# Kernel tuning notes

Hardware: AMD Instinct MI355X
Metric: run time of the kernel (lower is better)

## Reference

```python
import jax, jax.numpy as jnp
import numpy as np

KSIZE = 3
STRIDE = 1
PADDING = 1
DILATION = 1
C_IN = 16
C_OUT = 16


def setup_inputs() -> dict:
    key = jax.random.key(0)
    k1, k2, k3 = jax.random.split(key, 3)
    inputs = jax.random.normal(k1, (2, C_IN, 24, 24, 24, 24), dtype=jnp.float32)
    weight = jax.random.normal(k2, (C_OUT, C_IN * KSIZE ** 4), dtype=jnp.float32)
    bias = jax.random.normal(k3, (1, C_OUT, 1, 1, 1, 1), dtype=jnp.float32)
    return {"inputs": inputs, "weight": weight, "bias": bias}


def reference(inputs, weight, bias):
    # weight stored flattened: [C_out, C_in * k^4] -> [C_out, C_in, k, k, k, k]
    w = weight.reshape(C_OUT, C_IN, KSIZE, KSIZE, KSIZE, KSIZE)
    # General 4-spatial-dim convolution via XLA's ND conv.
    dn = jax.lax.ConvDimensionNumbers(
        lhs_spec=(0, 1, 2, 3, 4, 5),   # N, C, U, V, H, W
        rhs_spec=(0, 1, 2, 3, 4, 5),   # O, I, kU, kV, kH, kW
        out_spec=(0, 1, 2, 3, 4, 5),
    )
    out = jax.lax.conv_general_dilated(
        inputs, w,
        window_strides=(STRIDE,) * 4,
        padding=((PADDING, PADDING),) * 4,
        rhs_dilation=(DILATION,) * 4,
        dimension_numbers=dn,
    )
    return out + bias
```

## Files before the change

### kernel.cpp

```cpp
#include <hip/hip_runtime.h>

#define S 24
#define PLANE 576
#define CISTRIDE 331776
#define SLAB_B 21632
#define QBUF_B 6144
#define QOFF 3328
#define A_BYTES 46080
#define WS_SLABS A_BYTES

typedef __attribute__((ext_vector_type(8))) short bf16x8;
typedef __attribute__((ext_vector_type(4))) float f32x4;

__device__ __forceinline__ ushort f2bf(float f) {
    unsigned int u = __builtin_bit_cast(unsigned int, f);
    unsigned int r = u + 0x7fffu + ((u >> 16) & 1u);
    return (ushort)(r >> 16);
}

__global__ void __launch_bounds__(256)
pack_in(const float* __restrict__ in, const float* __restrict__ wgt, char* __restrict__ ws) {
    __shared__ __align__(16) float lds_f[16 * 576];

    const int b = blockIdx.x;
    const int nb = b / PLANE, uv = b % PLANE;
    const float* src = in + (size_t)nb * 16 * CISTRIDE + (size_t)uv * PLANE;
    char* dst = ws + WS_SLABS + (size_t)b * SLAB_B;
    const int t = threadIdx.x;

    #pragma unroll
    for (int r = 0; r < 9; ++r) {
        int chunk = r * 256 + t;
        int ci = chunk / 144, q4 = chunk % 144;
        __builtin_amdgcn_global_load_lds(
            (const __attribute__((address_space(1))) unsigned int*)(src + (size_t)ci * CISTRIDE + 4 * q4),
            (__attribute__((address_space(3))) unsigned int*)(&lds_f[chunk * 4]),
            16, 0, 0);
    }
    __syncthreads();

    #pragma unroll
    for (int i = 0; i < 6; ++i) {
        int c = i * 256 + t;
        if (c < 1352) {
            int pos = c >> 1, h = c & 1;
            int row = pos / 26, col = pos % 26;
            uint4 o = make_uint4(0, 0, 0, 0);
            if (row >= 1 && row <= 24 && col >= 1 && col <= 24) {
                int q = (row - 1) * 24 + (col - 1);
                #pragma unroll
                for (int kk = 0; kk < 4; ++kk) {
                    float fa = lds_f[(8 * h + 2 * kk) * 576 + q];
                    float fb = lds_f[(8 * h + 2 * kk + 1) * 576 + q];
                    ((unsigned*)&o)[kk] = (unsigned)f2bf(fa) | ((unsigned)f2bf(fb) << 16);
                }
            }
            *(uint4*)(dst + (((size_t)c * 16) ^ (size_t)((row & 3) << 4))) = o;
        }
    }

    if (b == 0) {
        for (int i = t; i < 2880; i += 256) {
            int step = i >> 6;
            int tap = step / 5, s = step % 5;
            int lane = i & 63;
            int co = lane & 15, gA = lane >> 4;
            int o = 2 * s + (gA >> 1);
            int cib = (gA & 1) * 8;
            ushort vals[8];
            #pragma unroll
            for (int j = 0; j < 8; ++j)
                vals[j] = (o <= 8) ? f2bf(wgt[co * 1296 + (cib + j) * 81 + tap * 9 + o]) : (ushort)0;
            uint4 pk;
            pk.x = vals[0] | ((unsigned)vals[1] << 16);
            pk.y = vals[2] | ((unsigned)vals[3] << 16);
            pk.z = vals[4] | ((unsigned)vals[5] << 16);
            pk.w = vals[6] | ((unsigned)vals[7] << 16);
            *(uint4*)(ws + (size_t)i * 16) = pk;
        }
    }
}

__global__ void __launch_bounds__(192, 4)
conv4d_main(const char* __restrict__ ws, const float* __restrict__ bias,
            float* __restrict__ out) {
    __shared__ __align__(16) char lds[2 * QBUF_B];

    const int t = threadIdx.x, lane = t & 63, wvid = t >> 6;
    const int braw = blockIdx.x;
    const int b = (braw & 7) * 216 + (braw >> 3);
    const int nb = b / 864, rem = b % 864;
    const int u = rem / 36, rem2 = rem % 36;
    const int v0 = (rem2 / 6) * 4, qq = rem2 % 6;

    const int n16 = lane & 15, g = lane >> 4;
    const int dh = n16 >> 3, dw = n16 & 7;
    const int half = g & 1, osel = g >> 1;

    int loff[2][5];
    #pragma unroll
    for (int tr = 0; tr < 2; ++tr)
        #pragma unroll
        for (int s = 0; s < 5; ++s) {
            int o = 2 * s + osel; if (o > 8) o = 8;
            int kh = o / 3, kw = o % 3;
            int r_off = dh + kh, c_off = dw + kw;
            int lin = (r_off * 26 + c_off) * 32 + half * 16;
            loff[tr][s] = lin ^ (((tr * 2 + r_off) & 3) << 4);
        }

    f32x4 acc[4][2];
    #pragma unroll
    for (int a = 0; a < 4; ++a)
        #pragma unroll
        for (int tr = 0; tr < 2; ++tr) acc[a][tr] = (f32x4){0, 0, 0, 0};

    unsigned mask = 0;
    #pragma unroll
    for (int i = 0; i < 18; ++i) {
        int uu = u + i / 6 - 1, vv = v0 + i % 6 - 1;
        if (uu >= 0 && uu < S && vv >= 0 && vv < S) mask |= 1u << i;
    }

    const char* slabs = ws + WS_SLABS;
    const size_t qoff = (size_t)qq * QOFF;
    #define SPTR(w_) (slabs + ((size_t)nb * PLANE                                        \
        + (size_t)min(max(u + (w_) / 6 - 1, 0), 23) * S                                  \
        + (size_t)min(max(v0 + (w_) % 6 - 1, 0), 23)) * SLAB_B + qoff)

    #define STAGE(bufsel_, src_) do {                                                    \
        const char* _s = (src_);                                                         \
        _Pragma("unroll")                                                                \
        for (int r2 = 0; r2 < 2; ++r2) {                                                 \
            int chunk = r2 * 192 + t;                                                    \
            __builtin_amdgcn_global_load_lds(                                            \
                (const __attribute__((address_space(1))) unsigned int*)(_s + (size_t)chunk * 16), \
                (__attribute__((address_space(3))) unsigned int*)(lds + (bufsel_) * QBUF_B + chunk * 16), \
                16, 0, 0);                                                               \
        }                                                                                \
    } while (0)

    STAGE(0, SPTR(0));
    STAGE(1, SPTR(1));

    bf16x8 afr[3][5];

    #pragma unroll
    for (int w = 0; w < 18; ++w) {
        if (w <= 16) asm volatile("s_waitcnt vmcnt(2)" ::: "memory");
        else         asm volatile("s_waitcnt vmcnt(0)" ::: "memory");
        __builtin_amdgcn_s_barrier();

        if ((w % 6) == 0) {
            const int ku = w / 6;
            #pragma unroll
            for (int kv = 0; kv < 3; ++kv) {
                const char* ap = ws + (size_t)(ku * 3 + kv) * 5120 + (size_t)lane * 16;
                #pragma unroll
                for (int s = 0; s < 5; ++s) afr[kv][s] = *(const bf16x8*)(ap + s * 1024);
            }
        }

        if (mask & (1u << w)) {
            const int vj = w % 6;
            const char* bp = lds + (w & 1) * QBUF_B + wvid * 256;
            #pragma unroll
            for (int tr = 0; tr < 2; ++tr) {
                #pragma unroll
                for (int s = 0; s < 5; ++s) {
                    bf16x8 bfr = *(const bf16x8*)(bp + tr * 1664 + loff[tr][s]);
                    #pragma unroll
                    for (int kv = 0; kv < 3; ++kv) {
                        const int a = vj - kv;
                        if (a >= 0 && a <= 3)
                            acc[a][tr] = __builtin_amdgcn_mfma_f32_16x16x32_bf16(afr[kv][s], bfr, acc[a][tr], 0, 0, 0);
                    }
                }
            }
        }
        __builtin_amdgcn_s_barrier();
        if (w + 2 < 18) STAGE(w & 1, SPTR(w + 2));
    }

    float bv[4];
    #pragma unroll
    for (int r = 0; r < 4; ++r) bv[r] = bias[g * 4 + r];
    #pragma unroll
    for (int a = 0; a < 4; ++a) {
        float* outp = out + (size_t)nb * 16 * CISTRIDE + (size_t)(u * S + v0 + a) * PLANE;
        #pragma unroll
        for (int tr = 0; tr < 2; ++tr) {
            int row = qq * 4 + tr * 2 + dh;
            int col = wvid * 8 + dw;
            int pos = row * S + col;
            #pragma unroll
            for (int r = 0; r < 4; ++r)
                outp[(size_t)(g * 4 + r) * CISTRIDE + pos] = acc[a][tr][r] + bv[r];
        }
    }
}

extern "C" void kernel_launch(void* const* d_in, const int* in_sizes, int n_in,
                              void* d_out, int out_size, void* d_ws, size_t ws_size,
                              hipStream_t stream) {
    const float* in   = (const float*)d_in[0];
    const float* wgt  = (const float*)d_in[1];
    const float* bias = (const float*)d_in[2];
    float* out        = (float*)d_out;
    char* ws          = (char*)d_ws;

    pack_in<<<dim3(1152), dim3(256), 0, stream>>>(in, wgt, ws);
    conv4d_main<<<dim3(1728), dim3(192), 0, stream>>>(ws, bias, out);
}
```

Measured before the change: 68.83 us.

## Fuse input bf16 packing into conv kernel, loading fp32 directly via registers

Drops the separate input-packing pass that wrote padded, swizzled bf16 slabs to workspace. The conv kernel now loads fp32 input straight from global memory into registers one window ahead, converts to bf16, writes the swizzled LDS tile itself and zero-fills the halo border. Only a tiny single-block kernel still packs the weights. This removes a full read-and-write pass over the input and one launch. In exchange the main kernel reads twice the bytes per element, prefetches only one stage ahead, and carries more registers.

```diff
diff --git a/kernel.cpp b/kernel.cpp
--- a/kernel.cpp
+++ b/kernel.cpp
@@ -3,11 +3,8 @@
 #define S 24
 #define PLANE 576
 #define CISTRIDE 331776
-#define SLAB_B 21632
-#define QBUF_B 6144
-#define QOFF 3328
+#define BUF_B 4992
 #define A_BYTES 46080
-#define WS_SLABS A_BYTES
 
 typedef __attribute__((ext_vector_type(8))) short bf16x8;
 typedef __attribute__((ext_vector_type(4))) float f32x4;
@@ -19,72 +16,32 @@
 }
 
 __global__ void __launch_bounds__(256)
-pack_in(const float* __restrict__ in, const float* __restrict__ wgt, char* __restrict__ ws) {
-    __shared__ __align__(16) float lds_f[16 * 576];
-
-    const int b = blockIdx.x;
-    const int nb = b / PLANE, uv = b % PLANE;
-    const float* src = in + (size_t)nb * 16 * CISTRIDE + (size_t)uv * PLANE;
-    char* dst = ws + WS_SLABS + (size_t)b * SLAB_B;
+pack_w(const float* __restrict__ wgt, char* __restrict__ ws) {
     const int t = threadIdx.x;
-
-    #pragma unroll
-    for (int r = 0; r < 9; ++r) {
-        int chunk = r * 256 + t;
-        int ci = chunk / 144, q4 = chunk % 144;
-        __builtin_amdgcn_global_load_lds(
-            (const __attribute__((address_space(1))) unsigned int*)(src + (size_t)ci * CISTRIDE + 4 * q4),
-            (__attribute__((address_space(3))) unsigned int*)(&lds_f[chunk * 4]),
-            16, 0, 0);
-    }
-    __syncthreads();
-
-    #pragma unroll
-    for (int i = 0; i < 6; ++i) {
-        int c = i * 256 + t;
-        if (c < 1352) {
-            int pos = c >> 1, h = c & 1;
-            int row = pos / 26, col = pos % 26;
-            uint4 o = make_uint4(0, 0, 0, 0);
-            if (row >= 1 && row <= 24 && col >= 1 && col <= 24) {
-                int q = (row - 1) * 24 + (col - 1);
-                #pragma unroll
-                for (int kk = 0; kk < 4; ++kk) {
-                    float fa = lds_f[(8 * h + 2 * kk) * 576 + q];
-                    float fb = lds_f[(8 * h + 2 * kk + 1) * 576 + q];
-                    ((unsigned*)&o)[kk] = (unsigned)f2bf(fa) | ((unsigned)f2bf(fb) << 16);
-                }
-            }
-            *(uint4*)(dst + (((size_t)c * 16) ^ (size_t)((row & 3) << 4))) = o;
-        }
-    }
-
-    if (b == 0) {
-        for (int i = t; i < 2880; i += 256) {
-            int step = i >> 6;
-            int tap = step / 5, s = step % 5;
-            int lane = i & 63;
-            int co = lane & 15, gA = lane >> 4;
-            int o = 2 * s + (gA >> 1);
-            int cib = (gA & 1) * 8;
-            ushort vals[8];
-            #pragma unroll
-            for (int j = 0; j < 8; ++j)
-                vals[j] = (o <= 8) ? f2bf(wgt[co * 1296 + (cib + j) * 81 + tap * 9 + o]) : (ushort)0;
-            uint4 pk;
-            pk.x = vals[0] | ((unsigned)vals[1] << 16);
-            pk.y = vals[2] | ((unsigned)vals[3] << 16);
-            pk.z = vals[4] | ((unsigned)vals[5] << 16);
-            pk.w = vals[6] | ((unsigned)vals[7] << 16);
-            *(uint4*)(ws + (size_t)i * 16) = pk;
-        }
+    for (int i = t; i < 2880; i += 256) {
+        int step = i >> 6;
+        int tap = step / 5, s = step % 5;
+        int lane = i & 63;
+        int co = lane & 15, gA = lane >> 4;
+        int o = 2 * s + (gA >> 1);
+        int cib = (gA & 1) * 8;
+        ushort vals[8];
+        #pragma unroll
+        for (int j = 0; j < 8; ++j)
+            vals[j] = (o <= 8) ? f2bf(wgt[co * 1296 + (cib + j) * 81 + tap * 9 + o]) : (ushort)0;
+        uint4 pk;
+        pk.x = vals[0] | ((unsigned)vals[1] << 16);
+        pk.y = vals[2] | ((unsigned)vals[3] << 16);
+        pk.z = vals[4] | ((unsigned)vals[5] << 16);
+        pk.w = vals[6] | ((unsigned)vals[7] << 16);
+        *(uint4*)(ws + (size_t)i * 16) = pk;
     }
 }
 
 __global__ void __launch_bounds__(192, 4)
-conv4d_main(const char* __restrict__ ws, const float* __restrict__ bias,
-            float* __restrict__ out) {
-    __shared__ __align__(16) char lds[2 * QBUF_B];
+conv4d_fused(const float* __restrict__ in, const char* __restrict__ ws,
+             const float* __restrict__ bias, float* __restrict__ out) {
+    __shared__ __align__(16) char lds[2 * BUF_B];
 
     const int t = threadIdx.x, lane = t & 63, wvid = t >> 6;
     const int braw = blockIdx.x;
@@ -122,34 +79,53 @@
         if (uu >= 0 && uu < S && vv >= 0 && vv < S) mask |= 1u << i;
     }
 
-    const char* slabs = ws + WS_SLABS;
-    const size_t qoff = (size_t)qq * QOFF;
-    #define SPTR(w_) (slabs + ((size_t)nb * PLANE                                        \
-        + (size_t)min(max(u + (w_) / 6 - 1, 0), 23) * S                                  \
-        + (size_t)min(max(v0 + (w_) % 6 - 1, 0), 23)) * SLAB_B + qoff)
+    const bool interior = t < 144;
+    const int l_row = interior ? t / 24 : 0;
+    const int c_in  = interior ? t % 24 : 0;
+    const int r_in  = 4 * qq + l_row - 1;
+    const bool rvalid = (r_in >= 0) && (r_in < 24);
+    const int rowcol = (rvalid ? r_in : 0) * 24 + c_in;
+    const int phase  = (l_row & 3) << 4;
+    const int wb_lo  = ((l_row * 26 + c_in + 1) * 32) ^ phase;
+    const int wb_hi  = ((l_row * 26 + c_in + 1) * 32 + 16) ^ phase;
+    const bool isborder = (t >= 144) && (t < 168);
+    const int bj = t - 144;
+    const int bl = bj / 4, bun = bj % 4;
+    const int bcol = (bun >> 1) ? 25 : 0, bh = bun & 1;
+    const int wbz = ((bl * 26 + bcol) * 32 + bh * 16) ^ ((bl & 3) << 4);
 
-    #define STAGE(bufsel_, src_) do {                                                    \
-        const char* _s = (src_);                                                         \
-        _Pragma("unroll")                                                                \
-        for (int r2 = 0; r2 < 2; ++r2) {                                                 \
-            int chunk = r2 * 192 + t;                                                    \
-            __builtin_amdgcn_global_load_lds(                                            \
-                (const __attribute__((address_space(1))) unsigned int*)(_s + (size_t)chunk * 16), \
-                (__attribute__((address_space(3))) unsigned int*)(lds + (bufsel_) * QBUF_B + chunk * 16), \
-                16, 0, 0);                                                               \
-        }                                                                                \
+    float fv[16];
+    #define LOADW(w_) do {                                                           \
+        const int _ku = (w_) / 6, _vj = (w_) % 6;                                    \
+        const int _uu = min(max(u + _ku - 1, 0), 23);                                \
+        const int _vv = min(max(v0 + _vj - 1, 0), 23);                               \
+        const bool _ok = interior && rvalid && ((mask >> (w_)) & 1u);                \
+        const float* _bp = in + (size_t)(nb * 16) * CISTRIDE                         \
+                              + (size_t)(_uu * S + _vv) * PLANE + rowcol;            \
+        _Pragma("unroll")                                                            \
+        for (int ci = 0; ci < 16; ++ci) fv[ci] = _ok ? _bp[(size_t)ci * CISTRIDE] : 0.f; \
     } while (0)
-
-    STAGE(0, SPTR(0));
-    STAGE(1, SPTR(1));
 
     bf16x8 afr[3][5];
 
+    LOADW(0);
+
     #pragma unroll
     for (int w = 0; w < 18; ++w) {
-        if (w <= 16) asm volatile("s_waitcnt vmcnt(2)" ::: "memory");
-        else         asm volatile("s_waitcnt vmcnt(0)" ::: "memory");
-        __builtin_amdgcn_s_barrier();
+        char* wbuf = lds + (w & 1) * BUF_B;
+        if (interior) {
+            unsigned pk[8];
+            #pragma unroll
+            for (int k = 0; k < 8; ++k)
+                pk[k] = (unsigned)f2bf(fv[2 * k]) | ((unsigned)f2bf(fv[2 * k + 1]) << 16);
+            *(uint4*)(wbuf + wb_lo) = make_uint4(pk[0], pk[1], pk[2], pk[3]);
+            *(uint4*)(wbuf + wb_hi) = make_uint4(pk[4], pk[5], pk[6], pk[7]);
+        } else if (isborder) {
+            *(uint4*)(wbuf + wbz) = make_uint4(0, 0, 0, 0);
+        }
+        __syncthreads();
+
+        if (w + 1 < 18) LOADW(w + 1);
 
         if ((w % 6) == 0) {
             const int ku = w / 6;
@@ -163,7 +139,7 @@
 
         if (mask & (1u << w)) {
             const int vj = w % 6;
-            const char* bp = lds + (w & 1) * QBUF_B + wvid * 256;
+            const char* bp = lds + (w & 1) * BUF_B + wvid * 256;
             #pragma unroll
             for (int tr = 0; tr < 2; ++tr) {
                 #pragma unroll
@@ -178,8 +154,6 @@
                 }
             }
         }
-        __builtin_amdgcn_s_barrier();
-        if (w + 2 < 18) STAGE(w & 1, SPTR(w + 2));
     }
 
     float bv[4];
@@ -209,6 +183,6 @@
     float* out        = (float*)d_out;
     char* ws          = (char*)d_ws;
 
-    pack_in<<<dim3(1152), dim3(256), 0, stream>>>(in, wgt, ws);
-    conv4d_main<<<dim3(1728), dim3(192), 0, stream>>>(ws, bias, out);
+    pack_w<<<dim3(1), dim3(256), 0, stream>>>(wgt, ws);
+    conv4d_fused<<<dim3(1728), dim3(192), 0, stream>>>(in, ws, bias, out);
 }
```

Measured after the change: 108.2 us. +57.2%, slower.
